# Kernel tuning notes

Hardware: AMD Instinct MI355X
Metric: run time of the kernel (lower is better)

## Reference

```python
import jax, jax.numpy as jnp
import numpy as np

NUM_HEADS = 8


def setup_inputs() -> dict:
    key = jax.random.key(0)
    ks = jax.random.split(key, 5)
    b, c, h, w = 8, 256, 32, 32
    x = jax.random.normal(ks[0], (b, c, h, w), dtype=jnp.float32)
    w_qkv = jax.random.normal(ks[1], (3 * c, c), dtype=jnp.float32) * (c ** -0.5)
    b_qkv = jax.random.normal(ks[2], (3 * c,), dtype=jnp.float32) * 0.02
    w_proj = jax.random.normal(ks[3], (c, c), dtype=jnp.float32) * (c ** -0.5)
    b_proj = jax.random.normal(ks[4], (c,), dtype=jnp.float32) * 0.02
    return {"x": x, "w_qkv": w_qkv, "b_qkv": b_qkv, "w_proj": w_proj, "b_proj": b_proj}


def reference(x, w_qkv, b_qkv, w_proj, b_proj):
    b, c, h, w = x.shape
    nh = NUM_HEADS
    dh = c // nh
    L = h * w
    scale = dh ** -0.5
    # 1x1 conv == per-pixel GEMM
    qkv = jnp.einsum('bchw,oc->bohw', x, w_qkv) + b_qkv[None, :, None, None]
    qkv = qkv.reshape(b, 3, nh, dh, L)
    q, k, v = qkv[:, 0], qkv[:, 1], qkv[:, 2]  # each (b, nh, dh, L)
    attn = jnp.einsum('bhdi,bhdj->bhij', q, k) * scale  # (b, nh, L, L)
    attn = jax.nn.softmax(attn, axis=-1)
    out = jnp.einsum('bhdj,bhij->bhdi', v, attn)  # (b, nh, dh, L)
    out = out.reshape(b, c, h, w)
    proj = jnp.einsum('bchw,oc->bohw', out, w_proj) + b_proj[None, :, None, None]
    return x + proj
```

## Files before the change

### kernel.cpp

```cpp
#include <hip/hip_runtime.h>
#include <math.h>

#define B_   8
#define CIN  256
#define L_   1024
#define NH_  8
#define DH_  32

typedef __attribute__((ext_vector_type(8))) short short8;
typedef __attribute__((ext_vector_type(4))) short short4v;
typedef __attribute__((ext_vector_type(4))) float f32x4;
typedef __attribute__((ext_vector_type(4))) unsigned int uint4v;
typedef __attribute__((ext_vector_type(2))) unsigned int uint2v;

__device__ inline short f2bf_hu(float f) {
    union { float f; unsigned u; } v; v.f = f;
    return (short)((v.u + 0x8000u) >> 16);
}
__device__ inline unsigned pkbf2(float a, float b) {
    union { float f; unsigned u; } x, y; x.f = a; y.f = b;
    return __builtin_amdgcn_perm(y.u + 0x8000u, x.u + 0x8000u, 0x07060302u);
}

__global__ __launch_bounds__(256) void transpose_cast(
    const float* __restrict__ x, short* __restrict__ xT)
{
    __shared__ short Ts[32][34];
    const int t = threadIdx.x;
    const int b = blockIdx.z, c0 = blockIdx.y * 32, l0 = blockIdx.x * 32;

    const int c = t >> 3, ls = (t & 7) * 4;
    const float4 x4 = *(const float4*)&x[(((size_t)b * CIN + c0 + c) << 10) + l0 + ls];
    Ts[ls + 0][c] = f2bf_hu(x4.x);
    Ts[ls + 1][c] = f2bf_hu(x4.y);
    Ts[ls + 2][c] = f2bf_hu(x4.z);
    Ts[ls + 3][c] = f2bf_hu(x4.w);
    __syncthreads();
    const int l = t >> 3, cs = (t & 7) * 4;
    uint2v o;
    o.x = (unsigned)(unsigned short)Ts[l][cs]     | ((unsigned)(unsigned short)Ts[l][cs + 1] << 16);
    o.y = (unsigned)(unsigned short)Ts[l][cs + 2] | ((unsigned)(unsigned short)Ts[l][cs + 3] << 16);
    *(uint2v*)&xT[(((size_t)b << 10) + l0 + l) * CIN + c0 + cs] = o;
}

__global__ __launch_bounds__(256) void qkv_gemm(
    const short* __restrict__ xT, const float* __restrict__ w,
    const float* __restrict__ bias, short* __restrict__ qkvT)
{
    __shared__ short Xs[64][40];
    __shared__ short Wt[128][40];
    const int t = threadIdx.x, lane = t & 63, wv = t >> 6;
    const int n = lane & 15, quad = lane >> 4;
    const int b = blockIdx.z, o0 = blockIdx.y * 128, l0 = blockIdx.x * 64;

    float bias_r[8];
    #pragma unroll
    for (int nf = 0; nf < 8; nf++) bias_r[nf] = bias[o0 + nf * 16 + n];

    f32x4 acc[8];
    #pragma unroll
    for (int nf = 0; nf < 8; nf++) acc[nf] = (f32x4){0.f, 0.f, 0.f, 0.f};

    for (int c0 = 0; c0 < CIN; c0 += 32) {
        {
            const int l = t >> 2, cs = (t & 3) * 8;
            *(uint4v*)&Xs[l][cs] =
                *(const uint4v*)&xT[(((size_t)b << 10) + l0 + l) * CIN + c0 + cs];
        }
        {
            const int o = t >> 1, cs = (t & 1) * 16;
            const float* wp = &w[(size_t)(o0 + o) * CIN + c0 + cs];
            const float4 w0 = *(const float4*)(wp);
            const float4 w1 = *(const float4*)(wp + 4);
            const float4 w2 = *(const float4*)(wp + 8);
            const float4 w3 = *(const float4*)(wp + 12);
            uint4v pa = { pkbf2(w0.x, w0.y), pkbf2(w0.z, w0.w),
                          pkbf2(w1.x, w1.y), pkbf2(w1.z, w1.w) };
            uint4v pb = { pkbf2(w2.x, w2.y), pkbf2(w2.z, w2.w),
                          pkbf2(w3.x, w3.y), pkbf2(w3.z, w3.w) };
            *(uint4v*)&Wt[o][cs]     = pa;
            *(uint4v*)&Wt[o][cs + 8] = pb;
        }
        __syncthreads();

        const short8 af = *(const short8*)&Xs[wv * 16 + n][quad * 8];
        #pragma unroll
        for (int nf = 0; nf < 8; nf++) {
            const short8 bf = *(const short8*)&Wt[nf * 16 + n][quad * 8];
            acc[nf] = __builtin_amdgcn_mfma_f32_16x16x32_bf16(af, bf, acc[nf], 0, 0, 0);
        }
        __syncthreads();
    }

    #pragma unroll
    for (int reg = 0; reg < 4; reg++) {
        const size_t l = l0 + wv * 16 + quad * 4 + reg;
        short* row = qkvT + (((size_t)b << 10) + l) * 768 + o0 + n;
        #pragma unroll
        for (int nf = 0; nf < 8; nf++)
            row[nf * 16] = f2bf_hu(acc[nf][reg] + bias_r[nf]);
    }
}

__global__ __launch_bounds__(256) void proj_gemm(
    const short* __restrict__ aT, const float* __restrict__ w,
    const float* __restrict__ bias, const float* __restrict__ resid,
    float* __restrict__ out)
{
    __shared__ short Xs[64][40];
    __shared__ short Wt[64][40];
    const int t = threadIdx.x, lane = t & 63, wv = t >> 6;
    const int n = lane & 15, quad = lane >> 4;
    const int b = blockIdx.z, o0 = blockIdx.y * 64, l0 = blockIdx.x * 64;

    float bias_r[4];
    #pragma unroll
    for (int reg = 0; reg < 4; reg++) bias_r[reg] = bias[o0 + wv * 16 + quad * 4 + reg];

    f32x4 acc[4];
    #pragma unroll
    for (int nf = 0; nf < 4; nf++) acc[nf] = (f32x4){0.f, 0.f, 0.f, 0.f};

    for (int c0 = 0; c0 < CIN; c0 += 32) {
        {
            const int l = t >> 2, cs = (t & 3) * 8;
            *(uint4v*)&Xs[l][cs] =
                *(const uint4v*)&aT[(((size_t)b << 10) + l0 + l) * CIN + c0 + cs];
        }
        {
            const int o = t >> 2, cs = (t & 3) * 8;
            const float* wp = &w[(size_t)(o0 + o) * CIN + c0 + cs];
            const float4 a4 = *(const float4*)(wp);
            const float4 b4 = *(const float4*)(wp + 4);
            uint4v pw = { pkbf2(a4.x, a4.y), pkbf2(a4.z, a4.w),
                          pkbf2(b4.x, b4.y), pkbf2(b4.z, b4.w) };
            *(uint4v*)&Wt[o][cs] = pw;
        }
        __syncthreads();

        const short8 af = *(const short8*)&Wt[wv * 16 + n][quad * 8];
        #pragma unroll
        for (int nf = 0; nf < 4; nf++) {
            const short8 bf = *(const short8*)&Xs[nf * 16 + n][quad * 8];
            acc[nf] = __builtin_amdgcn_mfma_f32_16x16x32_bf16(af, bf, acc[nf], 0, 0, 0);
        }
        __syncthreads();
    }

    #pragma unroll
    for (int reg = 0; reg < 4; reg++) {
        const int o = o0 + wv * 16 + quad * 4 + reg;
        #pragma unroll
        for (int nf = 0; nf < 4; nf++) {
            const size_t off = (((size_t)b * CIN + o) << 10) + l0 + nf * 16 + n;
            out[off] = acc[nf][reg] + bias_r[reg] + resid[off];
        }
    }
}

__global__ __launch_bounds__(256) void attn_mfma(
    const short* __restrict__ qkvT, short* __restrict__ attnoT)
{
    __shared__ short Ks[64][40];
    __shared__ short Vt[48][80];
    __shared__ __align__(16) char umem[64 * 80 * 2];
    short (*Ss)[80] = (short(*)[80])umem;
    float (*OtT)[38] = (float(*)[38])umem;

    const int t = threadIdx.x, lane = t & 63, wv = t >> 6;
    const int n = lane & 15, quad = lane >> 4;
    const int b = blockIdx.z, h = blockIdx.y, i0 = blockIdx.x * 64;

    const short* base = qkvT + ((size_t)b << 10) * 768;

    for (int idx = t; idx < 16 * 80; idx += 256) {
        const int r = idx / 80, c = idx - r * 80;
        Vt[32 + r][c] = (r == 0) ? (short)0x3F80 : (short)0;
    }

    const short8 qa = *(const short8*)&base[(size_t)(i0 + wv * 16 + n) * 768 + h * DH_ + quad * 8];

    f32x4 o_acc[3];
    #pragma unroll
    for (int nf = 0; nf < 3; nf++) o_acc[nf] = (f32x4){0.f, 0.f, 0.f, 0.f};

    const float K1 = 0.25503510f;
    const float K2 = 11.54156036f;

    for (int j0 = 0; j0 < L_; j0 += 64) {
        __syncthreads();
        {
            const int j = t >> 2, cs = (t & 3) * 8;
            *(uint4v*)&Ks[j][cs] =
                *(const uint4v*)&base[(size_t)(j0 + j) * 768 + 256 + h * DH_ + cs];
        }
        #pragma unroll
        for (int r = 0; r < 2; r++) {
            const int idx = t + r * 256;
            const int j = idx >> 3, ds = (idx & 7) * 4;
            const short4v v4 = *(const short4v*)&base[(size_t)(j0 + j) * 768 + 512 + h * DH_ + ds];
            #pragma unroll
            for (int u = 0; u < 4; u++) {
                const int dv = ds + u;
                Vt[dv][j ^ (((dv >> 2) & 7) << 3)] = v4[u];
            }
        }
        __syncthreads();

        #pragma unroll
        for (int f = 0; f < 4; f++) {
            const short8 kf = *(const short8*)&Ks[f * 16 + n][quad * 8];
            f32x4 z = {0.f, 0.f, 0.f, 0.f};
            const f32x4 s = __builtin_amdgcn_mfma_f32_16x16x32_bf16(kf, qa, z, 0, 0, 0);
            const float p0 = exp2f(fmaf(s[0], K1, -K2));
            const float p1 = exp2f(fmaf(s[1], K1, -K2));
            const float p2 = exp2f(fmaf(s[2], K1, -K2));
            const float p3 = exp2f(fmaf(s[3], K1, -K2));
            uint2v pk = { pkbf2(p0, p1), pkbf2(p2, p3) };
            *(uint2v*)&Ss[wv * 16 + n][f * 16 + quad * 4] = pk;
        }

        #pragma unroll
        for (int kk = 0; kk < 2; kk++) {
            const short8 pf = *(const short8*)&Ss[wv * 16 + n][kk * 32 + quad * 8];
            #pragma unroll
            for (int nf = 0; nf < 3; nf++) {
                const int dv = nf * 16 + n;
                const int msk = ((dv >> 2) & 7) << 3;
                const short8 vf = *(const short8*)&Vt[dv][(kk * 32 + quad * 8) ^ msk];
                o_acc[nf] = __builtin_amdgcn_mfma_f32_16x16x32_bf16(pf, vf, o_acc[nf], 0, 0, 0);
            }
        }
    }

    __syncthreads();
    #pragma unroll
    for (int r = 0; r < 4; r++) {
        const float lv  = __shfl(o_acc[2][r], lane & 48, 64);
        const float inv = 1.f / lv;
        const int il = wv * 16 + quad * 4 + r;
        OtT[il][n]      = o_acc[0][r] * inv;
        OtT[il][16 + n] = o_acc[1][r] * inv;
    }
    __syncthreads();
    short* ob = attnoT + (((size_t)b << 10) + i0) * CIN + h * DH_;
    #pragma unroll
    for (int r = 0; r < 2; r++) {
        const int idx = t + r * 256;
        const int l = idx >> 3, cs = (idx & 7) * 4;
        uint2v pv;
        pv.x = pkbf2(OtT[l][cs],     OtT[l][cs + 1]);
        pv.y = pkbf2(OtT[l][cs + 2], OtT[l][cs + 3]);
        *(uint2v*)&ob[(size_t)l * CIN + cs] = pv;
    }
}

extern "C" void kernel_launch(void* const* d_in, const int* in_sizes, int n_in,
                              void* d_out, int out_size, void* d_ws, size_t ws_size,
                              hipStream_t stream) {
    const float* x      = (const float*)d_in[0];
    const float* w_qkv  = (const float*)d_in[1];
    const float* b_qkv  = (const float*)d_in[2];
    const float* w_proj = (const float*)d_in[3];
    const float* b_proj = (const float*)d_in[4];
    float* out = (float*)d_out;

    short* xT     = (short*)d_ws;
    short* qkvT   = xT   + (size_t)B_ * L_ * CIN;
    short* attnoT = qkvT + (size_t)B_ * L_ * 768;

    transpose_cast<<<dim3(32, 8, B_), 256, 0, stream>>>(x, xT);
    qkv_gemm<<<dim3(16, 6, B_), 256, 0, stream>>>(xT, w_qkv, b_qkv, qkvT);
    attn_mfma<<<dim3(16, NH_, B_), 256, 0, stream>>>(qkvT, attnoT);
    proj_gemm<<<dim3(16, 4, B_), 256, 0, stream>>>(attnoT, w_proj, b_proj, x, out);
}
```

Measured before the change: 130.2 us.

## Fuse all stages into one persistent cooperative kernel with grid syncs

Replaces the four kernels (transpose-cast, QKV GEMM, attention, projection) with one persistent cooperative kernel whose phases are separated by grid.sync. The QKV GEMM now reads fp32 x directly with strided per-element loads and converts weights in registers, with no LDS staging. This drops the xT intermediate and the per-launch gaps. In exchange, the GEMM phases lose LDS tiling and reuse, issue many scattered global loads, and pay for two grid-wide barriers.

```diff
diff --git a/kernel.cpp b/kernel.cpp
--- a/kernel.cpp
+++ b/kernel.cpp
@@ -1,5 +1,8 @@
 #include <hip/hip_runtime.h>
+#include <hip/hip_cooperative_groups.h>
 #include <math.h>
+
+namespace cg = cooperative_groups;
 
 #define B_   8
 #define CIN  256
@@ -22,236 +25,184 @@
     return __builtin_amdgcn_perm(y.u + 0x8000u, x.u + 0x8000u, 0x07060302u);
 }
 
-__global__ __launch_bounds__(256) void transpose_cast(
-    const float* __restrict__ x, short* __restrict__ xT)
-{
-    __shared__ short Ts[32][34];
-    const int t = threadIdx.x;
-    const int b = blockIdx.z, c0 = blockIdx.y * 32, l0 = blockIdx.x * 32;
-
-    const int c = t >> 3, ls = (t & 7) * 4;
-    const float4 x4 = *(const float4*)&x[(((size_t)b * CIN + c0 + c) << 10) + l0 + ls];
-    Ts[ls + 0][c] = f2bf_hu(x4.x);
-    Ts[ls + 1][c] = f2bf_hu(x4.y);
-    Ts[ls + 2][c] = f2bf_hu(x4.z);
-    Ts[ls + 3][c] = f2bf_hu(x4.w);
-    __syncthreads();
-    const int l = t >> 3, cs = (t & 7) * 4;
-    uint2v o;
-    o.x = (unsigned)(unsigned short)Ts[l][cs]     | ((unsigned)(unsigned short)Ts[l][cs + 1] << 16);
-    o.y = (unsigned)(unsigned short)Ts[l][cs + 2] | ((unsigned)(unsigned short)Ts[l][cs + 3] << 16);
-    *(uint2v*)&xT[(((size_t)b << 10) + l0 + l) * CIN + c0 + cs] = o;
-}
-
-__global__ __launch_bounds__(256) void qkv_gemm(
-    const short* __restrict__ xT, const float* __restrict__ w,
-    const float* __restrict__ bias, short* __restrict__ qkvT)
-{
-    __shared__ short Xs[64][40];
-    __shared__ short Wt[128][40];
-    const int t = threadIdx.x, lane = t & 63, wv = t >> 6;
-    const int n = lane & 15, quad = lane >> 4;
-    const int b = blockIdx.z, o0 = blockIdx.y * 128, l0 = blockIdx.x * 64;
-
-    float bias_r[8];
-    #pragma unroll
-    for (int nf = 0; nf < 8; nf++) bias_r[nf] = bias[o0 + nf * 16 + n];
-
-    f32x4 acc[8];
-    #pragma unroll
-    for (int nf = 0; nf < 8; nf++) acc[nf] = (f32x4){0.f, 0.f, 0.f, 0.f};
-
-    for (int c0 = 0; c0 < CIN; c0 += 32) {
-        {
-            const int l = t >> 2, cs = (t & 3) * 8;
-            *(uint4v*)&Xs[l][cs] =
-                *(const uint4v*)&xT[(((size_t)b << 10) + l0 + l) * CIN + c0 + cs];
-        }
-        {
-            const int o = t >> 1, cs = (t & 1) * 16;
-            const float* wp = &w[(size_t)(o0 + o) * CIN + c0 + cs];
-            const float4 w0 = *(const float4*)(wp);
-            const float4 w1 = *(const float4*)(wp + 4);
-            const float4 w2 = *(const float4*)(wp + 8);
-            const float4 w3 = *(const float4*)(wp + 12);
-            uint4v pa = { pkbf2(w0.x, w0.y), pkbf2(w0.z, w0.w),
-                          pkbf2(w1.x, w1.y), pkbf2(w1.z, w1.w) };
-            uint4v pb = { pkbf2(w2.x, w2.y), pkbf2(w2.z, w2.w),
-                          pkbf2(w3.x, w3.y), pkbf2(w3.z, w3.w) };
-            *(uint4v*)&Wt[o][cs]     = pa;
-            *(uint4v*)&Wt[o][cs + 8] = pb;
-        }
-        __syncthreads();
-
-        const short8 af = *(const short8*)&Xs[wv * 16 + n][quad * 8];
-        #pragma unroll
-        for (int nf = 0; nf < 8; nf++) {
-            const short8 bf = *(const short8*)&Wt[nf * 16 + n][quad * 8];
-            acc[nf] = __builtin_amdgcn_mfma_f32_16x16x32_bf16(af, bf, acc[nf], 0, 0, 0);
-        }
-        __syncthreads();
-    }
-
-    #pragma unroll
-    for (int reg = 0; reg < 4; reg++) {
-        const size_t l = l0 + wv * 16 + quad * 4 + reg;
-        short* row = qkvT + (((size_t)b << 10) + l) * 768 + o0 + n;
-        #pragma unroll
-        for (int nf = 0; nf < 8; nf++)
-            row[nf * 16] = f2bf_hu(acc[nf][reg] + bias_r[nf]);
-    }
-}
-
-__global__ __launch_bounds__(256) void proj_gemm(
-    const short* __restrict__ aT, const float* __restrict__ w,
-    const float* __restrict__ bias, const float* __restrict__ resid,
-    float* __restrict__ out)
-{
-    __shared__ short Xs[64][40];
-    __shared__ short Wt[64][40];
-    const int t = threadIdx.x, lane = t & 63, wv = t >> 6;
-    const int n = lane & 15, quad = lane >> 4;
-    const int b = blockIdx.z, o0 = blockIdx.y * 64, l0 = blockIdx.x * 64;
-
-    float bias_r[4];
-    #pragma unroll
-    for (int reg = 0; reg < 4; reg++) bias_r[reg] = bias[o0 + wv * 16 + quad * 4 + reg];
-
-    f32x4 acc[4];
-    #pragma unroll
-    for (int nf = 0; nf < 4; nf++) acc[nf] = (f32x4){0.f, 0.f, 0.f, 0.f};
-
-    for (int c0 = 0; c0 < CIN; c0 += 32) {
-        {
-            const int l = t >> 2, cs = (t & 3) * 8;
-            *(uint4v*)&Xs[l][cs] =
-                *(const uint4v*)&aT[(((size_t)b << 10) + l0 + l) * CIN + c0 + cs];
-        }
-        {
-            const int o = t >> 2, cs = (t & 3) * 8;
-            const float* wp = &w[(size_t)(o0 + o) * CIN + c0 + cs];
-            const float4 a4 = *(const float4*)(wp);
-            const float4 b4 = *(const float4*)(wp + 4);
-            uint4v pw = { pkbf2(a4.x, a4.y), pkbf2(a4.z, a4.w),
-                          pkbf2(b4.x, b4.y), pkbf2(b4.z, b4.w) };
-            *(uint4v*)&Wt[o][cs] = pw;
-        }
-        __syncthreads();
-
-        const short8 af = *(const short8*)&Wt[wv * 16 + n][quad * 8];
-        #pragma unroll
-        for (int nf = 0; nf < 4; nf++) {
-            const short8 bf = *(const short8*)&Xs[nf * 16 + n][quad * 8];
-            acc[nf] = __builtin_amdgcn_mfma_f32_16x16x32_bf16(af, bf, acc[nf], 0, 0, 0);
-        }
-        __syncthreads();
-    }
-
-    #pragma unroll
-    for (int reg = 0; reg < 4; reg++) {
-        const int o = o0 + wv * 16 + quad * 4 + reg;
-        #pragma unroll
-        for (int nf = 0; nf < 4; nf++) {
-            const size_t off = (((size_t)b * CIN + o) << 10) + l0 + nf * 16 + n;
-            out[off] = acc[nf][reg] + bias_r[reg] + resid[off];
-        }
-    }
-}
-
-__global__ __launch_bounds__(256) void attn_mfma(
-    const short* __restrict__ qkvT, short* __restrict__ attnoT)
+__global__ __launch_bounds__(256, 4) void mega(
+    const float* __restrict__ x,      const float* __restrict__ w_qkv,
+    const float* __restrict__ b_qkv,  const float* __restrict__ w_proj,
+    const float* __restrict__ b_proj, float* __restrict__ out,
+    short* __restrict__ qkvT,         short* __restrict__ attnoT)
 {
     __shared__ short Ks[64][40];
     __shared__ short Vt[48][80];
     __shared__ __align__(16) char umem[64 * 80 * 2];
-    short (*Ss)[80] = (short(*)[80])umem;
+    short (*Ss)[80]  = (short(*)[80])umem;
     float (*OtT)[38] = (float(*)[38])umem;
 
+    cg::grid_group grid = cg::this_grid();
     const int t = threadIdx.x, lane = t & 63, wv = t >> 6;
     const int n = lane & 15, quad = lane >> 4;
-    const int b = blockIdx.z, h = blockIdx.y, i0 = blockIdx.x * 64;
-
-    const short* base = qkvT + ((size_t)b << 10) * 768;
+    const int nblk = gridDim.x;
+
+    for (int it = blockIdx.x; it < 1024; it += nblk) {
+        const int b = it >> 7, r = it & 127;
+        const int o0 = (r >> 4) * 96, l0 = (r & 15) * 64;
+
+        f32x4 acc[6];
+        #pragma unroll
+        for (int nf = 0; nf < 6; nf++) acc[nf] = (f32x4){0.f, 0.f, 0.f, 0.f};
+
+        for (int c0 = 0; c0 < CIN; c0 += 32) {
+            const float* xp = x + (((size_t)(b * CIN + c0 + quad * 8)) << 10)
+                                + l0 + wv * 16 + n;
+            short8 af;
+            #pragma unroll
+            for (int u = 0; u < 8; u++) af[u] = f2bf_hu(xp[(size_t)u << 10]);
+
+            #pragma unroll
+            for (int nf = 0; nf < 6; nf++) {
+                const float* wp = w_qkv + (size_t)(o0 + nf * 16 + n) * CIN + c0 + quad * 8;
+                const float4 w0 = *(const float4*)wp;
+                const float4 w1 = *(const float4*)(wp + 4);
+                union { uint4v u; short8 s; } bfu;
+                bfu.u = (uint4v){ pkbf2(w0.x, w0.y), pkbf2(w0.z, w0.w),
+                                  pkbf2(w1.x, w1.y), pkbf2(w1.z, w1.w) };
+                acc[nf] = __builtin_amdgcn_mfma_f32_16x16x32_bf16(af, bfu.s, acc[nf], 0, 0, 0);
+            }
+        }
+        #pragma unroll
+        for (int nf = 0; nf < 6; nf++) {
+            const int o = o0 + nf * 16 + n;
+            const float bi = b_qkv[o];
+            #pragma unroll
+            for (int reg = 0; reg < 4; reg++) {
+                const size_t l = l0 + wv * 16 + quad * 4 + reg;
+                qkvT[(((size_t)b << 10) + l) * 768 + o] = f2bf_hu(acc[nf][reg] + bi);
+            }
+        }
+    }
+
+    grid.sync();
 
     for (int idx = t; idx < 16 * 80; idx += 256) {
-        const int r = idx / 80, c = idx - r * 80;
-        Vt[32 + r][c] = (r == 0) ? (short)0x3F80 : (short)0;
-    }
-
-    const short8 qa = *(const short8*)&base[(size_t)(i0 + wv * 16 + n) * 768 + h * DH_ + quad * 8];
-
-    f32x4 o_acc[3];
-    #pragma unroll
-    for (int nf = 0; nf < 3; nf++) o_acc[nf] = (f32x4){0.f, 0.f, 0.f, 0.f};
+        const int rr = idx / 80, c = idx - rr * 80;
+        Vt[32 + rr][c] = (rr == 0) ? (short)0x3F80 : (short)0;
+    }
 
     const float K1 = 0.25503510f;
     const float K2 = 11.54156036f;
 
-    for (int j0 = 0; j0 < L_; j0 += 64) {
+    for (int it = blockIdx.x; it < 1024; it += nblk) {
+        const int b = it >> 7, h = (it >> 4) & 7, i0 = (it & 15) * 64;
+        const short* base = qkvT + (((size_t)b << 10)) * 768;
+
+        const short8 qa = *(const short8*)&base[(size_t)(i0 + wv * 16 + n) * 768
+                                                + h * DH_ + quad * 8];
+        f32x4 o_acc[3];
+        #pragma unroll
+        for (int nf = 0; nf < 3; nf++) o_acc[nf] = (f32x4){0.f, 0.f, 0.f, 0.f};
+
+        for (int j0 = 0; j0 < L_; j0 += 64) {
+            __syncthreads();
+            {
+                const int j = t >> 2, cs = (t & 3) * 8;
+                *(uint4v*)&Ks[j][cs] =
+                    *(const uint4v*)&base[(size_t)(j0 + j) * 768 + 256 + h * DH_ + cs];
+            }
+            #pragma unroll
+            for (int rr = 0; rr < 2; rr++) {
+                const int idx = t + rr * 256;
+                const int j = idx >> 3, ds = (idx & 7) * 4;
+                const short4v v4 = *(const short4v*)&base[(size_t)(j0 + j) * 768
+                                                          + 512 + h * DH_ + ds];
+                #pragma unroll
+                for (int u = 0; u < 4; u++) {
+                    const int dv = ds + u;
+                    Vt[dv][j ^ (((dv >> 2) & 7) << 3)] = v4[u];
+                }
+            }
+            __syncthreads();
+
+            #pragma unroll
+            for (int f = 0; f < 4; f++) {
+                const short8 kf = *(const short8*)&Ks[f * 16 + n][quad * 8];
+                f32x4 z = {0.f, 0.f, 0.f, 0.f};
+                const f32x4 s = __builtin_amdgcn_mfma_f32_16x16x32_bf16(kf, qa, z, 0, 0, 0);
+                const float p0 = exp2f(fmaf(s[0], K1, -K2));
+                const float p1 = exp2f(fmaf(s[1], K1, -K2));
+                const float p2 = exp2f(fmaf(s[2], K1, -K2));
+                const float p3 = exp2f(fmaf(s[3], K1, -K2));
+                uint2v pk = { pkbf2(p0, p1), pkbf2(p2, p3) };
+                *(uint2v*)&Ss[wv * 16 + n][f * 16 + quad * 4] = pk;
+            }
+
+            #pragma unroll
+            for (int kk = 0; kk < 2; kk++) {
+                const short8 pf = *(const short8*)&Ss[wv * 16 + n][kk * 32 + quad * 8];
+                #pragma unroll
+                for (int nf = 0; nf < 3; nf++) {
+                    const int dv = nf * 16 + n;
+                    const int msk = ((dv >> 2) & 7) << 3;
+                    const short8 vf = *(const short8*)&Vt[dv][(kk * 32 + quad * 8) ^ msk];
+                    o_acc[nf] = __builtin_amdgcn_mfma_f32_16x16x32_bf16(pf, vf, o_acc[nf], 0, 0, 0);
+                }
+            }
+        }
+
         __syncthreads();
-        {
-            const int j = t >> 2, cs = (t & 3) * 8;
-            *(uint4v*)&Ks[j][cs] =
-                *(const uint4v*)&base[(size_t)(j0 + j) * 768 + 256 + h * DH_ + cs];
-        }
-        #pragma unroll
-        for (int r = 0; r < 2; r++) {
-            const int idx = t + r * 256;
-            const int j = idx >> 3, ds = (idx & 7) * 4;
-            const short4v v4 = *(const short4v*)&base[(size_t)(j0 + j) * 768 + 512 + h * DH_ + ds];
-            #pragma unroll
-            for (int u = 0; u < 4; u++) {
-                const int dv = ds + u;
-                Vt[dv][j ^ (((dv >> 2) & 7) << 3)] = v4[u];
-            }
+        #pragma unroll
+        for (int rr = 0; rr < 4; rr++) {
+            const float lv  = __shfl(o_acc[2][rr], lane & 48, 64);
+            const float inv = 1.f / lv;
+            const int il = wv * 16 + quad * 4 + rr;
+            OtT[il][n]      = o_acc[0][rr] * inv;
+            OtT[il][16 + n] = o_acc[1][rr] * inv;
         }
         __syncthreads();
-
-        #pragma unroll
-        for (int f = 0; f < 4; f++) {
-            const short8 kf = *(const short8*)&Ks[f * 16 + n][quad * 8];
-            f32x4 z = {0.f, 0.f, 0.f, 0.f};
-            const f32x4 s = __builtin_amdgcn_mfma_f32_16x16x32_bf16(kf, qa, z, 0, 0, 0);
-            const float p0 = exp2f(fmaf(s[0], K1, -K2));
-            const float p1 = exp2f(fmaf(s[1], K1, -K2));
-            const float p2 = exp2f(fmaf(s[2], K1, -K2));
-            const float p3 = exp2f(fmaf(s[3], K1, -K2));
-            uint2v pk = { pkbf2(p0, p1), pkbf2(p2, p3) };
-            *(uint2v*)&Ss[wv * 16 + n][f * 16 + quad * 4] = pk;
-        }
-
-        #pragma unroll
-        for (int kk = 0; kk < 2; kk++) {
-            const short8 pf = *(const short8*)&Ss[wv * 16 + n][kk * 32 + quad * 8];
-            #pragma unroll
-            for (int nf = 0; nf < 3; nf++) {
-                const int dv = nf * 16 + n;
-                const int msk = ((dv >> 2) & 7) << 3;
-                const short8 vf = *(const short8*)&Vt[dv][(kk * 32 + quad * 8) ^ msk];
-                o_acc[nf] = __builtin_amdgcn_mfma_f32_16x16x32_bf16(pf, vf, o_acc[nf], 0, 0, 0);
-            }
-        }
-    }
-
-    __syncthreads();
-    #pragma unroll
-    for (int r = 0; r < 4; r++) {
-        const float lv  = __shfl(o_acc[2][r], lane & 48, 64);
-        const float inv = 1.f / lv;
-        const int il = wv * 16 + quad * 4 + r;
-        OtT[il][n]      = o_acc[0][r] * inv;
-        OtT[il][16 + n] = o_acc[1][r] * inv;
-    }
-    __syncthreads();
-    short* ob = attnoT + (((size_t)b << 10) + i0) * CIN + h * DH_;
-    #pragma unroll
-    for (int r = 0; r < 2; r++) {
-        const int idx = t + r * 256;
-        const int l = idx >> 3, cs = (idx & 7) * 4;
-        uint2v pv;
-        pv.x = pkbf2(OtT[l][cs],     OtT[l][cs + 1]);
-        pv.y = pkbf2(OtT[l][cs + 2], OtT[l][cs + 3]);
-        *(uint2v*)&ob[(size_t)l * CIN + cs] = pv;
+        short* ob = attnoT + ((((size_t)b << 10)) + i0) * CIN + h * DH_;
+        #pragma unroll
+        for (int rr = 0; rr < 2; rr++) {
+            const int idx = t + rr * 256;
+            const int l = idx >> 3, cs = (idx & 7) * 4;
+            uint2v pv;
+            pv.x = pkbf2(OtT[l][cs],     OtT[l][cs + 1]);
+            pv.y = pkbf2(OtT[l][cs + 2], OtT[l][cs + 3]);
+            *(uint2v*)&ob[(size_t)l * CIN + cs] = pv;
+        }
+    }
+
+    grid.sync();
+
+    for (int it = blockIdx.x; it < 1024; it += nblk) {
+        const int b = it >> 7, r = it & 127;
+        const int o0 = (r >> 5) * 64, l0 = (r & 31) * 32;
+
+        f32x4 acc[2];
+        #pragma unroll
+        for (int nf = 0; nf < 2; nf++) acc[nf] = (f32x4){0.f, 0.f, 0.f, 0.f};
+
+        for (int c0 = 0; c0 < CIN; c0 += 32) {
+            const float* wp = w_proj + (size_t)(o0 + wv * 16 + n) * CIN + c0 + quad * 8;
+            const float4 w0 = *(const float4*)wp;
+            const float4 w1 = *(const float4*)(wp + 4);
+            union { uint4v u; short8 s; } afu;
+            afu.u = (uint4v){ pkbf2(w0.x, w0.y), pkbf2(w0.z, w0.w),
+                              pkbf2(w1.x, w1.y), pkbf2(w1.z, w1.w) };
+            #pragma unroll
+            for (int nf = 0; nf < 2; nf++) {
+                const short8 bf = *(const short8*)&attnoT[
+                    (((size_t)b << 10) + l0 + nf * 16 + n) * CIN + c0 + quad * 8];
+                acc[nf] = __builtin_amdgcn_mfma_f32_16x16x32_bf16(afu.s, bf, acc[nf], 0, 0, 0);
+            }
+        }
+        #pragma unroll
+        for (int reg = 0; reg < 4; reg++) {
+            const int o = o0 + wv * 16 + quad * 4 + reg;
+            const float bi = b_proj[o];
+            #pragma unroll
+            for (int nf = 0; nf < 2; nf++) {
+                const size_t off = (((size_t)b * CIN + o) << 10) + l0 + nf * 16 + n;
+                out[off] = acc[nf][reg] + bi + x[off];
+            }
+        }
     }
 }
 
@@ -263,14 +214,19 @@
     const float* b_qkv  = (const float*)d_in[2];
     const float* w_proj = (const float*)d_in[3];
     const float* b_proj = (const float*)d_in[4];
-    float* out = (float*)d_out;
-
-    short* xT     = (short*)d_ws;
-    short* qkvT   = xT   + (size_t)B_ * L_ * CIN;
+    float* outp = (float*)d_out;
+
+    short* qkvT   = (short*)d_ws;
     short* attnoT = qkvT + (size_t)B_ * L_ * 768;
 
-    transpose_cast<<<dim3(32, 8, B_), 256, 0, stream>>>(x, xT);
-    qkv_gemm<<<dim3(16, 6, B_), 256, 0, stream>>>(xT, w_qkv, b_qkv, qkvT);
-    attn_mfma<<<dim3(16, NH_, B_), 256, 0, stream>>>(qkvT, attnoT);
-    proj_gemm<<<dim3(16, 4, B_), 256, 0, stream>>>(attnoT, w_proj, b_proj, x, out);
-}
+    int occ = 0;
+    hipOccupancyMaxActiveBlocksPerMultiprocessor(&occ, mega, 256, 0);
+    if (occ < 1) occ = 1;
+    unsigned int nblk = (unsigned int)occ * 256u;
+    if (nblk > 1024u) nblk = 1024u;
+
+    void* args[] = { (void*)&x, (void*)&w_qkv, (void*)&b_qkv, (void*)&w_proj,
+                     (void*)&b_proj, (void*)&outp, (void*)&qkvT, (void*)&attnoT };
+    hipLaunchCooperativeKernel((const void*)mega, dim3(nblk), dim3(256),
+                               args, 0, stream);
+}
```

Measured after the change: 309.1 us. 2.37x slower.

## Fuse transpose into QKV GEMM and double-buffer attention K/V loads

Applied to the files above, without the earlier changes.

Removes the separate transpose/cast kernel by loading fp32 x directly in the QKV GEMM, converting to bf16 and writing a swizzled LDS tile. The attention kernel now keeps K fragments in registers with next-tile prefetch, double-buffers V in LDS to drop one barrier per iteration, and uses a register constant for the row-sum MFMA instead of LDS ones rows. This trades extra registers and more scattered global reads in the GEMM for fewer launches and less sync stall.

```diff
diff --git a/kernel.cpp b/kernel.cpp
--- a/kernel.cpp
+++ b/kernel.cpp
@@ -22,29 +22,8 @@
     return __builtin_amdgcn_perm(y.u + 0x8000u, x.u + 0x8000u, 0x07060302u);
 }
 
-__global__ __launch_bounds__(256) void transpose_cast(
-    const float* __restrict__ x, short* __restrict__ xT)
-{
-    __shared__ short Ts[32][34];
-    const int t = threadIdx.x;
-    const int b = blockIdx.z, c0 = blockIdx.y * 32, l0 = blockIdx.x * 32;
-
-    const int c = t >> 3, ls = (t & 7) * 4;
-    const float4 x4 = *(const float4*)&x[(((size_t)b * CIN + c0 + c) << 10) + l0 + ls];
-    Ts[ls + 0][c] = f2bf_hu(x4.x);
-    Ts[ls + 1][c] = f2bf_hu(x4.y);
-    Ts[ls + 2][c] = f2bf_hu(x4.z);
-    Ts[ls + 3][c] = f2bf_hu(x4.w);
-    __syncthreads();
-    const int l = t >> 3, cs = (t & 7) * 4;
-    uint2v o;
-    o.x = (unsigned)(unsigned short)Ts[l][cs]     | ((unsigned)(unsigned short)Ts[l][cs + 1] << 16);
-    o.y = (unsigned)(unsigned short)Ts[l][cs + 2] | ((unsigned)(unsigned short)Ts[l][cs + 3] << 16);
-    *(uint2v*)&xT[(((size_t)b << 10) + l0 + l) * CIN + c0 + cs] = o;
-}
-
 __global__ __launch_bounds__(256) void qkv_gemm(
-    const short* __restrict__ xT, const float* __restrict__ w,
+    const float* __restrict__ x, const float* __restrict__ w,
     const float* __restrict__ bias, short* __restrict__ qkvT)
 {
     __shared__ short Xs[64][40];
@@ -61,11 +40,21 @@
     #pragma unroll
     for (int nf = 0; nf < 8; nf++) acc[nf] = (f32x4){0.f, 0.f, 0.f, 0.f};
 
+    const int cS = t >> 3, lsS = (t & 7) * 8;
+    const int rslot = ((cS >> 3) << 3) | (cS & 7);
+
     for (int c0 = 0; c0 < CIN; c0 += 32) {
         {
-            const int l = t >> 2, cs = (t & 3) * 8;
-            *(uint4v*)&Xs[l][cs] =
-                *(const uint4v*)&xT[(((size_t)b << 10) + l0 + l) * CIN + c0 + cs];
+            const float* xp = &x[(((size_t)b * CIN + c0 + cS) << 10) + l0 + lsS];
+            const float4 xa = *(const float4*)xp;
+            const float4 xb = *(const float4*)(xp + 4);
+            const float vals[8] = {xa.x, xa.y, xa.z, xa.w, xb.x, xb.y, xb.z, xb.w};
+            #pragma unroll
+            for (int k = 0; k < 8; k++) {
+                const int l = lsS + k;
+                const int col = (((cS >> 3) ^ (l & 3)) << 3) | (cS & 7);
+                Xs[l][col] = f2bf_hu(vals[k]);
+            }
         }
         {
             const int o = t >> 1, cs = (t & 1) * 16;
@@ -83,7 +72,8 @@
         }
         __syncthreads();
 
-        const short8 af = *(const short8*)&Xs[wv * 16 + n][quad * 8];
+        const int arow = wv * 16 + n;
+        const short8 af = *(const short8*)&Xs[arow][(quad ^ (arow & 3)) * 8];
         #pragma unroll
         for (int nf = 0; nf < 8; nf++) {
             const short8 bf = *(const short8*)&Wt[nf * 16 + n][quad * 8];
@@ -161,10 +151,9 @@
 __global__ __launch_bounds__(256) void attn_mfma(
     const short* __restrict__ qkvT, short* __restrict__ attnoT)
 {
-    __shared__ short Ks[64][40];
-    __shared__ short Vt[48][80];
-    __shared__ __align__(16) char umem[64 * 80 * 2];
-    short (*Ss)[80] = (short(*)[80])umem;
+    __shared__ short Vt[2][32][80];
+    __shared__ __align__(16) char umem[64 * 88 * 2];
+    short (*Ss)[88] = (short(*)[88])umem;
     float (*OtT)[38] = (float(*)[38])umem;
 
     const int t = threadIdx.x, lane = t & 63, wv = t >> 6;
@@ -172,13 +161,17 @@
     const int b = blockIdx.z, h = blockIdx.y, i0 = blockIdx.x * 64;
 
     const short* base = qkvT + ((size_t)b << 10) * 768;
-
-    for (int idx = t; idx < 16 * 80; idx += 256) {
-        const int r = idx / 80, c = idx - r * 80;
-        Vt[32 + r][c] = (r == 0) ? (short)0x3F80 : (short)0;
-    }
+    const short* kbase = base + 256 + h * DH_;
+    const short* vbase = base + 512 + h * DH_;
 
     const short8 qa = *(const short8*)&base[(size_t)(i0 + wv * 16 + n) * 768 + h * DH_ + quad * 8];
+
+    short8 vf2;
+    {
+        const short one = (n == 0) ? (short)0x3F80 : (short)0;
+        #pragma unroll
+        for (int u = 0; u < 8; u++) vf2[u] = one;
+    }
 
     f32x4 o_acc[3];
     #pragma unroll
@@ -187,31 +180,49 @@
     const float K1 = 0.25503510f;
     const float K2 = 11.54156036f;
 
-    for (int j0 = 0; j0 < L_; j0 += 64) {
-        __syncthreads();
-        {
-            const int j = t >> 2, cs = (t & 3) * 8;
-            *(uint4v*)&Ks[j][cs] =
-                *(const uint4v*)&base[(size_t)(j0 + j) * 768 + 256 + h * DH_ + cs];
-        }
-        #pragma unroll
-        for (int r = 0; r < 2; r++) {
-            const int idx = t + r * 256;
-            const int j = idx >> 3, ds = (idx & 7) * 4;
-            const short4v v4 = *(const short4v*)&base[(size_t)(j0 + j) * 768 + 512 + h * DH_ + ds];
-            #pragma unroll
-            for (int u = 0; u < 4; u++) {
-                const int dv = ds + u;
-                Vt[dv][j ^ (((dv >> 2) & 7) << 3)] = v4[u];
+    const int jS = t >> 3, dsS = (t & 7) * 4;
+
+    #pragma unroll
+    for (int rr = 0; rr < 2; rr++) {
+        const int j = jS + rr * 32;
+        const short4v v4 = *(const short4v*)&vbase[(size_t)j * 768 + dsS];
+        #pragma unroll
+        for (int u = 0; u < 4; u++) {
+            const int dv = dsS + u;
+            Vt[0][dv][j ^ (((dv >> 2) & 7) << 3)] = v4[u];
+        }
+    }
+    short8 kf[4];
+    #pragma unroll
+    for (int f = 0; f < 4; f++)
+        kf[f] = *(const short8*)&kbase[(size_t)(f * 16 + n) * 768 + quad * 8];
+
+    for (int it = 0; it < 16; it++) {
+        const int cur = it & 1;
+        __syncthreads();
+
+        short8 kf_n[4];
+        if (it < 15) {
+            const int j0n = (it + 1) * 64;
+            #pragma unroll
+            for (int rr = 0; rr < 2; rr++) {
+                const int j = jS + rr * 32;
+                const short4v v4 = *(const short4v*)&vbase[(size_t)(j0n + j) * 768 + dsS];
+                #pragma unroll
+                for (int u = 0; u < 4; u++) {
+                    const int dv = dsS + u;
+                    Vt[cur ^ 1][dv][j ^ (((dv >> 2) & 7) << 3)] = v4[u];
+                }
             }
-        }
-        __syncthreads();
+            #pragma unroll
+            for (int f = 0; f < 4; f++)
+                kf_n[f] = *(const short8*)&kbase[(size_t)(j0n + f * 16 + n) * 768 + quad * 8];
+        }
 
         #pragma unroll
         for (int f = 0; f < 4; f++) {
-            const short8 kf = *(const short8*)&Ks[f * 16 + n][quad * 8];
             f32x4 z = {0.f, 0.f, 0.f, 0.f};
-            const f32x4 s = __builtin_amdgcn_mfma_f32_16x16x32_bf16(kf, qa, z, 0, 0, 0);
+            const f32x4 s = __builtin_amdgcn_mfma_f32_16x16x32_bf16(kf[f], qa, z, 0, 0, 0);
             const float p0 = exp2f(fmaf(s[0], K1, -K2));
             const float p1 = exp2f(fmaf(s[1], K1, -K2));
             const float p2 = exp2f(fmaf(s[2], K1, -K2));
@@ -224,13 +235,17 @@
         for (int kk = 0; kk < 2; kk++) {
             const short8 pf = *(const short8*)&Ss[wv * 16 + n][kk * 32 + quad * 8];
             #pragma unroll
-            for (int nf = 0; nf < 3; nf++) {
+            for (int nf = 0; nf < 2; nf++) {
                 const int dv = nf * 16 + n;
                 const int msk = ((dv >> 2) & 7) << 3;
-                const short8 vf = *(const short8*)&Vt[dv][(kk * 32 + quad * 8) ^ msk];
+                const short8 vf = *(const short8*)&Vt[cur][dv][(kk * 32 + quad * 8) ^ msk];
                 o_acc[nf] = __builtin_amdgcn_mfma_f32_16x16x32_bf16(pf, vf, o_acc[nf], 0, 0, 0);
             }
-        }
+            o_acc[2] = __builtin_amdgcn_mfma_f32_16x16x32_bf16(pf, vf2, o_acc[2], 0, 0, 0);
+        }
+
+        #pragma unroll
+        for (int f = 0; f < 4; f++) kf[f] = kf_n[f];
     }
 
     __syncthreads();
@@ -265,12 +280,10 @@
     const float* b_proj = (const float*)d_in[4];
     float* out = (float*)d_out;
 
-    short* xT     = (short*)d_ws;
-    short* qkvT   = xT   + (size_t)B_ * L_ * CIN;
+    short* qkvT   = (short*)d_ws;
     short* attnoT = qkvT + (size_t)B_ * L_ * 768;
 
-    transpose_cast<<<dim3(32, 8, B_), 256, 0, stream>>>(x, xT);
-    qkv_gemm<<<dim3(16, 6, B_), 256, 0, stream>>>(xT, w_qkv, b_qkv, qkvT);
+    qkv_gemm<<<dim3(16, 6, B_), 256, 0, stream>>>(x, w_qkv, b_qkv, qkvT);
     attn_mfma<<<dim3(16, NH_, B_), 256, 0, stream>>>(qkvT, attnoT);
     proj_gemm<<<dim3(16, 4, B_), 256, 0, stream>>>(attnoT, w_proj, b_proj, x, out);
 }
```

Result: no change. 129.6 us (-0.5%).
